# Performance work log

Measured on AMD Instinct MI355X. Metric: run time of the kernel, lower is better.

## Reference

```python
import jax, jax.numpy as jnp
import numpy as np

B, T, C, H = 16, 2048, 512, 4
DH = C // H  # head dim = 128


def setup_inputs() -> dict:
    key = jax.random.key(0)
    ks = jax.random.split(key, 12)
    s = 1.0 / np.sqrt(C).astype(np.float32)
    u = lambda k, shape: jax.random.uniform(k, shape, jnp.float32, -s, s)
    return {
        "x": jax.random.normal(ks[0], (B, C, 2, T), jnp.float32),
        "device_embedding": jax.random.normal(ks[1], (1, 2, C), jnp.float32),
        "in_proj_w": u(ks[2], (3 * C, C)),
        "in_proj_b": jnp.zeros((3 * C,), jnp.float32),
        "out_proj_w": u(ks[3], (C, C)),
        "out_proj_b": jnp.zeros((C,), jnp.float32),
        "phone_w": u(ks[4], (C, C)),
        "phone_b": u(ks[5], (C,)),
        "imu_w": u(ks[6], (C, C)),
        "imu_b": u(ks[7], (C,)),
        "output_w": u(ks[8], (C, 2 * C)),
        "output_b": u(ks[9], (C,)),
    }


def reference(x, device_embedding, in_proj_w, in_proj_b, out_proj_w, out_proj_b,
              phone_w, phone_b, imu_w, imu_b, output_w, output_b):
    Bx, Cx, Hdev, Tx = x.shape  # Hdev == 2 devices (phone, IMU)
    N = Bx * Tx
    # (B, C, 2, T) -> (B*T, 2, C), add learned device embedding
    xe = jnp.transpose(x, (0, 3, 2, 1)).reshape(N, 2, Cx) + device_embedding
    # torch nn.MultiheadAttention: packed in_proj, scale 1/sqrt(head_dim)
    wq, wk, wv = jnp.split(in_proj_w, 3, axis=0)
    bq, bk, bv = jnp.split(in_proj_b, 3, axis=0)
    to_heads = lambda t: t.reshape(N, 2, H, DH).transpose(0, 2, 1, 3)  # (N, H, 2, DH)
    q = to_heads(xe @ wq.T + bq)
    k = to_heads(xe @ wk.T + bk)
    v = to_heads(xe @ wv.T + bv)
    scores = jnp.einsum('nhqd,nhkd->nhqk', q, k) / jnp.float32(np.sqrt(DH))
    probs = jax.nn.softmax(scores, axis=-1)  # (N, H, 2, 2)
    ctx = jnp.einsum('nhqk,nhkd->nhqd', probs, v).transpose(0, 2, 1, 3).reshape(N, 2, Cx)
    attended = (ctx @ out_proj_w.T + out_proj_b).reshape(Bx, Tx, 2, Cx)
    phone = attended[:, :, 0, :] @ phone_w.T + phone_b
    imu = attended[:, :, 1, :] @ imu_w.T + imu_b
    out = jnp.concatenate([phone, imu], axis=-1) @ output_w.T + output_b  # (B, T, C)
    out = jnp.transpose(out, (0, 2, 1))  # (B, C, T)
    # head-averaged attention weights, then averaged over time
    avg_attention = probs.mean(axis=1).reshape(Bx, Tx, 2, 2).mean(axis=1)  # (B, 2, 2)
    return out, avg_attention
```

## Files before the change

kernel.cpp:

```cpp
#include <hip/hip_runtime.h>
#include <stdint.h>

typedef unsigned short u16;
typedef short short8 __attribute__((ext_vector_type(8)));
typedef float floatx4 __attribute__((ext_vector_type(4)));

__device__ __forceinline__ u16 f2bf(float f) {
  union { float f; unsigned u; } t; t.f = f;
  return (u16)((t.u + 0x7fffu + ((t.u >> 16) & 1u)) >> 16);
}
__device__ __forceinline__ float lo16(unsigned w) { union { unsigned u; float f; } t; t.u = w << 16; return t.f; }
__device__ __forceinline__ float hi16(unsigned w) { union { unsigned u; float f; } t; t.u = w & 0xffff0000u; return t.f; }
__device__ __forceinline__ void unpack8(uint4 v, float* f) {
  f[0]=lo16(v.x); f[1]=hi16(v.x); f[2]=lo16(v.y); f[3]=hi16(v.y);
  f[4]=lo16(v.z); f[5]=hi16(v.z); f[6]=lo16(v.w); f[7]=hi16(v.w);
}
__device__ __forceinline__ uint4 pack8(const u16* o) {
  uint4 v;
  v.x = (unsigned)o[0] | ((unsigned)o[1] << 16);
  v.y = (unsigned)o[2] | ((unsigned)o[3] << 16);
  v.z = (unsigned)o[4] | ((unsigned)o[5] << 16);
  v.w = (unsigned)o[6] | ((unsigned)o[7] << 16);
  return v;
}

__device__ __forceinline__ void gll16(const void* g, void* l) {
  __builtin_amdgcn_global_load_lds(
      (const __attribute__((address_space(1))) void*)(uintptr_t)(g),
      (__attribute__((address_space(3))) void*)(unsigned)(uintptr_t)(l),
      16, 0, 0);
}

__device__ __forceinline__ void cvt4(const float* s, u16* d, int g) {
  float4 v = *(const float4*)(s + (size_t)g * 4);
  ushort4 o; o.x = f2bf(v.x); o.y = f2bf(v.y); o.z = f2bf(v.z); o.w = f2bf(v.w);
  *(ushort4*)(d + (size_t)g * 4) = o;
}
__global__ __launch_bounds__(256)
void prep_convert(const float* __restrict__ inw, const float* __restrict__ phw,
                  const float* __restrict__ imw, const float* __restrict__ ow,
                  const float* __restrict__ outw,
                  u16* __restrict__ inw_bf, u16* __restrict__ phw_bf,
                  u16* __restrict__ imw_bf, u16* __restrict__ ow_bf,
                  u16* __restrict__ outwT) {
  int which = blockIdx.y;
  int g = blockIdx.x * 256 + threadIdx.x;
  if (which == 0) { if (g < 196608) cvt4(inw, inw_bf, g); }
  else if (which == 1) { if (g < 65536) cvt4(phw, phw_bf, g); }
  else if (which == 2) { if (g < 65536) cvt4(imw, imw_bf, g); }
  else if (which == 3) { if (g < 131072) cvt4(ow, ow_bf, g); }
  else {
    if (g < 65536) {
      int i0 = (g >> 9) * 4, j = g & 511;
      ushort4 o;
      o.x = f2bf(outw[(size_t)(i0 + 0) * 512 + j]);
      o.y = f2bf(outw[(size_t)(i0 + 1) * 512 + j]);
      o.z = f2bf(outw[(size_t)(i0 + 2) * 512 + j]);
      o.w = f2bf(outw[(size_t)(i0 + 3) * 512 + j]);
      outwT[(size_t)j * 512 + i0 + 0] = o.x;
      outwT[(size_t)j * 512 + i0 + 1] = o.y;
      outwT[(size_t)j * 512 + i0 + 2] = o.z;
      outwT[(size_t)j * 512 + i0 + 3] = o.w;
    }
  }
}

__global__ __launch_bounds__(256)
void uv_kernel(const float* __restrict__ phw, const float* __restrict__ phb,
               const float* __restrict__ imw, const float* __restrict__ imb,
               const float* __restrict__ outb, float* __restrict__ uv) {
  int g = blockIdx.x * 256 + threadIdx.x;
  int i = g & 511;
  const float* W = (g < 512) ? phw : imw;
  const float* bb = (g < 512) ? phb : imb;
  float s = bb[i];
#pragma unroll 4
  for (int c = 0; c < 512; ++c) s += W[(size_t)i * 512 + c] * outb[c];
  uv[g] = s;
}

__global__ __launch_bounds__(256)
void bcomb_kernel(const float* __restrict__ ow, const float* __restrict__ ob,
                  const float* __restrict__ uv, float* __restrict__ bcomb) {
  int i = blockIdx.x * 256 + threadIdx.x;
  float s = ob[i];
#pragma unroll 4
  for (int r = 0; r < 1024; ++r) s += ow[(size_t)i * 1024 + r] * uv[r];
  bcomb[i] = s;
}

__global__ __launch_bounds__(256)
void build_xe(const float* __restrict__ x, const float* __restrict__ emb,
              u16* __restrict__ xe) {
  __shared__ u16 tile[64][66];
  int bt = blockIdx.x;
  int tt = bt & 31, ct = (bt >> 5) & 7, d = (bt >> 8) & 1, b = bt >> 9;
  int t0 = tt * 64, c0 = ct * 64;
  int tid = threadIdx.x;
  int q = tid & 15, r = tid >> 4;
#pragma unroll
  for (int p = 0; p < 4; ++p) {
    int c = p * 16 + r;
    const float* src = x + ((size_t)((b * 512 + c0 + c) * 2 + d)) * 2048 + t0 + q * 4;
    float4 v = *(const float4*)src;
    float e = emb[d * 512 + c0 + c];
    ushort4 o; o.x = f2bf(v.x + e); o.y = f2bf(v.y + e); o.z = f2bf(v.z + e); o.w = f2bf(v.w + e);
    *(ushort4*)&tile[c][q * 4] = o;
  }
  __syncthreads();
  int cq = tid & 7, tp = tid >> 3;
  int cc0 = cq * 8;
  u16 o0[8], o1[8];
#pragma unroll
  for (int i = 0; i < 8; ++i) {
    unsigned w2 = *(const unsigned*)&tile[cc0 + i][2 * tp];
    o0[i] = (u16)(w2 & 0xffffu); o1[i] = (u16)(w2 >> 16);
  }
  size_t n = (size_t)b * 2048 + t0 + 2 * tp;
  *(uint4*)(xe + (n * 2 + d) * 512 + c0 + cc0) = pack8(o0);
  *(uint4*)(xe + ((n + 1) * 2 + d) * 512 + c0 + cc0) = pack8(o1);
}

template<int EPI>
__global__ __launch_bounds__(256, 3)
void gemm_bt(const u16* __restrict__ A, int lda,
             const u16* __restrict__ B, int ldb,
             const float* __restrict__ bias,
             void* __restrict__ Cv, int ldc, int K,
             const float* __restrict__ P) {
  __shared__ u16 As[128 * 64];
  __shared__ u16 Bs[128 * 64];
  int m0 = blockIdx.x * 128;
  int n0 = blockIdx.y * 128;
  int t = threadIdx.x;
  int lane = t & 63;
  int w = t >> 6;
  int wm = (w >> 1) * 64, wn = (w & 1) * 64;
  int l15 = lane & 15, quad = lane >> 4;

  floatx4 acc[4][4];
#pragma unroll
  for (int i = 0; i < 4; ++i)
#pragma unroll
    for (int j = 0; j < 4; ++j) acc[i][j] = (floatx4){0.f, 0.f, 0.f, 0.f};

  int lrow = lane >> 3, lcol = (lane & 7) * 8;
  const u16* gA = A + (size_t)(m0 + w * 32 + lrow) * lda + lcol;
  const u16* gB = B + (size_t)(n0 + w * 32 + lrow) * ldb + lcol;
  u16* lA = As + (w * 32) * 64;
  u16* lB = Bs + (w * 32) * 64;

  int KT = K >> 6;
  for (int kt = 0; kt < KT; ++kt) {
    int ko = kt * 64;
#pragma unroll
    for (int j = 0; j < 4; ++j) {
      gll16(gA + (size_t)(j * 8) * lda + ko, lA + (j * 8) * 64);
      gll16(gB + (size_t)(j * 8) * ldb + ko, lB + (j * 8) * 64);
    }
    __syncthreads();
#pragma unroll
    for (int ki = 0; ki < 2; ++ki) {
      short8 af[4], bfv[4];
#pragma unroll
      for (int i = 0; i < 4; ++i)
        af[i] = *(const short8*)&As[(wm + i * 16 + l15) * 64 + ki * 32 + quad * 8];
#pragma unroll
      for (int j = 0; j < 4; ++j)
        bfv[j] = *(const short8*)&Bs[(wn + j * 16 + l15) * 64 + ki * 32 + quad * 8];
#pragma unroll
      for (int i = 0; i < 4; ++i)
#pragma unroll
        for (int j = 0; j < 4; ++j)
          acc[i][j] = __builtin_amdgcn_mfma_f32_16x16x32_bf16(af[i], bfv[j], acc[i][j], 0, 0, 0);
    }
    __syncthreads();
  }

#pragma unroll
  for (int i = 0; i < 4; ++i) {
    int mrow = m0 + wm + i * 16 + quad * 4;
    float4 P0, P1;
    if (EPI == 2) {
      int np0 = mrow >> 1;
      P0 = *(const float4*)&P[((size_t)np0 * 4 + blockIdx.y) * 4];
      P1 = *(const float4*)&P[((size_t)(np0 + 1) * 4 + blockIdx.y) * 4];
    }
#pragma unroll
    for (int j = 0; j < 4; ++j) {
      int col = n0 + wn + j * 16 + l15;
      float bv = bias[col];
      floatx4 a = acc[i][j];
      if (EPI == 1) {
        int bb = mrow >> 11, ti = mrow & 2047;
        float4 o; o.x = a[0] + bv; o.y = a[1] + bv; o.z = a[2] + bv; o.w = a[3] + bv;
        *(float4*)&((float*)Cv)[((size_t)bb * ldc + col) * 2048 + ti] = o;
      } else if (EPI == 2) {
        float a0 = a[0] + bv, a1 = a[1] + bv, a2 = a[2] + bv, a3 = a[3] + bv;
        u16* C = (u16*)Cv;
        C[(size_t)(mrow + 0) * ldc + col] = f2bf(P0.x * a0 + P0.y * a1);
        C[(size_t)(mrow + 1) * ldc + col] = f2bf(P0.z * a0 + P0.w * a1);
        C[(size_t)(mrow + 2) * ldc + col] = f2bf(P1.x * a2 + P1.y * a3);
        C[(size_t)(mrow + 3) * ldc + col] = f2bf(P1.z * a2 + P1.w * a3);
      } else {
        u16* C = (u16*)Cv;
#pragma unroll
        for (int r = 0; r < 4; ++r)
          C[(size_t)(mrow + r) * ldc + col] = f2bf(a[r] + bv);
      }
    }
  }
}

__device__ __forceinline__ void compute_tile(const u16 (&Asr)[4][8192],
                                             const u16 (&Bsr)[4][8192],
                                             int bo, int aoff, int boff,
                                             floatx4 (&acc)[8][4]) {
  short8 af[8], bfv[4];
#pragma unroll
  for (int i = 0; i < 8; ++i)
    af[i] = *(const short8*)&Asr[bo][aoff + i * 512];
#pragma unroll
  for (int j = 0; j < 4; ++j)
    bfv[j] = *(const short8*)&Bsr[bo][boff + j * 512];
  __builtin_amdgcn_s_setprio(1);
#pragma unroll
  for (int i = 0; i < 8; ++i)
#pragma unroll
    for (int j = 0; j < 4; ++j)
      acc[i][j] = __builtin_amdgcn_mfma_f32_16x16x32_bf16(af[i], bfv[j], acc[i][j], 0, 0, 0);
  __builtin_amdgcn_s_setprio(0);
}

template<int EPI>
__global__ __launch_bounds__(512, 2)
void gemm256(const u16* __restrict__ A, int lda,
             const u16* __restrict__ B, int ldb,
             const float* __restrict__ bias,
             void* __restrict__ Cv, int ldc, int K,
             const float* __restrict__ P, int nbs) {
  __shared__ u16 As[4][8192];
  __shared__ u16 Bs[4][8192];
  int nwg = gridDim.x;
  int bid = blockIdx.x;
  int chunk = nwg >> 3;
  int g = (bid & 7) * chunk + (bid >> 3);
  int nb = g & ((1 << nbs) - 1), mb = g >> nbs;
  int m0 = mb * 256, n0 = nb * 256;
  int t = threadIdx.x;
  int lane = t & 63, w = t >> 6;
  int wr = w >> 2, wc = w & 3;
  int l15 = lane & 15, quad = lane >> 4;
  int wb = w * 512;
  int srow = t >> 2, sch = (t & 3) * 8;
  const u16* gA0 = A + (size_t)(m0 + srow) * lda + sch;
  const u16* gA1 = gA0 + (size_t)128 * lda;
  const u16* gB0 = B + (size_t)(n0 + srow) * ldb + sch;
  const u16* gB1 = gB0 + (size_t)128 * ldb;

  floatx4 acc[8][4];
#pragma unroll
  for (int i = 0; i < 8; ++i)
#pragma unroll
    for (int j = 0; j < 4; ++j) acc[i][j] = (floatx4){0.f, 0.f, 0.f, 0.f};

  int aoff = (wr * 128 + l15) * 32 + quad * 8;
  int boff = (wc * 64 + l15) * 32 + quad * 8;
  int KT = K >> 5;

#define STAGE256(ts) { int _b = (ts) & 3; int _ko = (ts) * 32;             \
    gll16(gA0 + _ko, (void*)&As[_b][wb]);                                  \
    gll16(gA1 + _ko, (void*)&As[_b][wb + 4096]);                           \
    gll16(gB0 + _ko, (void*)&Bs[_b][wb]);                                  \
    gll16(gB1 + _ko, (void*)&Bs[_b][wb + 4096]); }

  STAGE256(0)
  STAGE256(1)
  STAGE256(2)
  for (int tt = 0; tt < KT - 3; ++tt) {
    STAGE256(tt + 3)
    asm volatile("s_waitcnt vmcnt(12)" ::: "memory");
    asm volatile("s_barrier" ::: "memory");
    compute_tile(As, Bs, tt & 3, aoff, boff, acc);
    asm volatile("s_barrier" ::: "memory");
  }
  asm volatile("s_waitcnt vmcnt(8)" ::: "memory");
  asm volatile("s_barrier" ::: "memory");
  compute_tile(As, Bs, (KT - 3) & 3, aoff, boff, acc);
  asm volatile("s_waitcnt vmcnt(4)" ::: "memory");
  asm volatile("s_barrier" ::: "memory");
  compute_tile(As, Bs, (KT - 2) & 3, aoff, boff, acc);
  asm volatile("s_waitcnt vmcnt(0)" ::: "memory");
  asm volatile("s_barrier" ::: "memory");
  compute_tile(As, Bs, (KT - 1) & 3, aoff, boff, acc);
#undef STAGE256

#pragma unroll
  for (int i = 0; i < 8; ++i) {
    int mrow = m0 + wr * 128 + i * 16 + quad * 4;
#pragma unroll
    for (int j = 0; j < 4; ++j) {
      int col = n0 + wc * 64 + j * 16 + l15;
      float bv = bias[col];
      floatx4 a = acc[i][j];
      if (EPI == 1) {
        int bb = mrow >> 11, ti = mrow & 2047;
        float4 o; o.x = a[0] + bv; o.y = a[1] + bv; o.z = a[2] + bv; o.w = a[3] + bv;
        *(float4*)&((float*)Cv)[((size_t)bb * ldc + col) * 2048 + ti] = o;
      } else if (EPI == 2) {
        int np0 = mrow >> 1;
        int h = col >> 7;
        float4 P0 = *(const float4*)&P[((size_t)np0 * 4 + h) * 4];
        float4 P1 = *(const float4*)&P[((size_t)(np0 + 1) * 4 + h) * 4];
        float a0 = a[0] + bv, a1 = a[1] + bv, a2 = a[2] + bv, a3 = a[3] + bv;
        u16* C = (u16*)Cv;
        C[(size_t)(mrow + 0) * ldc + col] = f2bf(P0.x * a0 + P0.y * a1);
        C[(size_t)(mrow + 1) * ldc + col] = f2bf(P0.z * a0 + P0.w * a1);
        C[(size_t)(mrow + 2) * ldc + col] = f2bf(P1.x * a2 + P1.y * a3);
        C[(size_t)(mrow + 3) * ldc + col] = f2bf(P1.z * a2 + P1.w * a3);
      } else {
        u16* C = (u16*)Cv;
#pragma unroll
        for (int r = 0; r < 4; ++r)
          C[(size_t)(mrow + r) * ldc + col] = f2bf(a[r] + bv);
      }
    }
  }
}

__global__ __launch_bounds__(256)
void score_kernel(const u16* __restrict__ QK, float* __restrict__ P,
                  float* __restrict__ asum) {
  int g = blockIdx.x * 256 + threadIdx.x;
  int n = g >> 2, h = g & 3;
  const u16* q0 = QK + (size_t)(2 * n) * 1024 + h * 128;
  const u16* q1 = q0 + 1024;
  const u16* k0 = q0 + 512;
  const u16* k1 = k0 + 1024;

  float s00 = 0.f, s01 = 0.f, s10 = 0.f, s11 = 0.f;
#pragma unroll
  for (int c = 0; c < 128; c += 8) {
    float fq0[8], fq1[8], fk0[8], fk1[8];
    unpack8(*(const uint4*)(q0 + c), fq0);
    unpack8(*(const uint4*)(q1 + c), fq1);
    unpack8(*(const uint4*)(k0 + c), fk0);
    unpack8(*(const uint4*)(k1 + c), fk1);
#pragma unroll
    for (int u = 0; u < 8; ++u) {
      s00 += fq0[u] * fk0[u]; s01 += fq0[u] * fk1[u];
      s10 += fq1[u] * fk0[u]; s11 += fq1[u] * fk1[u];
    }
  }
  const float sc = 0.08838834764831845f;
  s00 *= sc; s01 *= sc; s10 *= sc; s11 *= sc;
  float m0v = fmaxf(s00, s01), m1v = fmaxf(s10, s11);
  float e00 = __expf(s00 - m0v), e01 = __expf(s01 - m0v);
  float e10 = __expf(s10 - m1v), e11 = __expf(s11 - m1v);
  float i0 = 1.f / (e00 + e01), i1 = 1.f / (e10 + e11);
  float4 p; p.x = e00 * i0; p.y = e01 * i0; p.z = e10 * i1; p.w = e11 * i1;
  *(float4*)&P[(size_t)g * 4] = p;

  float pv[4] = {p.x, p.y, p.z, p.w};
#pragma unroll
  for (int k2 = 0; k2 < 4; ++k2) {
    float v = pv[k2];
    v += __shfl_down(v, 32, 64); v += __shfl_down(v, 16, 64);
    v += __shfl_down(v, 8, 64);  v += __shfl_down(v, 4, 64);
    v += __shfl_down(v, 2, 64);  v += __shfl_down(v, 1, 64);
    pv[k2] = v;
  }
  __shared__ float red[4][4];
  int lane = threadIdx.x & 63, wv = threadIdx.x >> 6;
  if (lane == 0) { red[wv][0] = pv[0]; red[wv][1] = pv[1]; red[wv][2] = pv[2]; red[wv][3] = pv[3]; }
  __syncthreads();
  if (threadIdx.x < 4) {
    float s = red[0][threadIdx.x] + red[1][threadIdx.x] + red[2][threadIdx.x] + red[3][threadIdx.x];
    int b = (blockIdx.x * 64) >> 11;
    atomicAdd(&asum[b * 4 + threadIdx.x], s);
  }
}

__global__ void avg_kernel(const float* __restrict__ asum, float* __restrict__ out) {
  int i = threadIdx.x;
  out[16777216 + i] = asum[i] * (1.0f / 8192.0f);
}

extern "C" void kernel_launch(void* const* d_in, const int* in_sizes, int n_in,
                              void* d_out, int out_size, void* d_ws, size_t ws_size,
                              hipStream_t stream) {
  const float* x    = (const float*)d_in[0];
  const float* emb  = (const float*)d_in[1];
  const float* inw  = (const float*)d_in[2];
  const float* inb  = (const float*)d_in[3];
  const float* outw = (const float*)d_in[4];
  const float* outb = (const float*)d_in[5];
  const float* phw  = (const float*)d_in[6];
  const float* phb  = (const float*)d_in[7];
  const float* imw  = (const float*)d_in[8];
  const float* imb  = (const float*)d_in[9];
  const float* ow   = (const float*)d_in[10];
  const float* ob   = (const float*)d_in[11];
  float* outF = (float*)d_out;

  char* wsb = (char*)d_ws;
  u16*   ctx    = (u16*)wsb;
  u16*   QK     = (u16*)(wsb + 67108864);
  u16*   outwT  = (u16*)(wsb + 67108864);
  u16*   phw_bf = (u16*)(wsb + 67633152);
  u16*   imw_bf = (u16*)(wsb + 68157440);
  u16*   ow_bf  = (u16*)(wsb + 68681728);
  u16*   T1T    = (u16*)(wsb + 69730304);
  u16*   T2T    = (u16*)(wsb + 70254592);
  u16*   inw_bf = (u16*)(wsb + 201326592);
  u16*   Wcomb  = (u16*)(wsb + 202899456);
  float* uv     = (float*)(wsb + 203948032);
  float* bcomb  = (float*)(wsb + 203952128);
  float* P      = (float*)(wsb + 203954176);
  float* asum   = (float*)(wsb + 206051328);
  float* zbias  = (float*)(wsb + 206051584);
  u16*   xe     = (u16*)d_out;

  hipMemsetAsync(asum, 0, 2304, stream);

  build_xe<<<8192, 256, 0, stream>>>(x, emb, xe);

  prep_convert<<<dim3(768, 5), 256, 0, stream>>>(inw, phw, imw, ow, outw,
                                                 inw_bf, phw_bf, imw_bf, ow_bf, outwT);
  gemm_bt<0><<<dim3(4, 4), 256, 0, stream>>>(outwT, 512, phw_bf, 512, zbias, T1T, 512, 512, nullptr);
  gemm_bt<0><<<dim3(4, 4), 256, 0, stream>>>(outwT, 512, imw_bf, 512, zbias, T2T, 512, 512, nullptr);
  gemm_bt<0><<<dim3(4, 4), 256, 0, stream>>>(ow_bf, 1024, T1T, 512, zbias, Wcomb, 1024, 512, nullptr);
  gemm_bt<0><<<dim3(4, 4), 256, 0, stream>>>(ow_bf + 512, 1024, T2T, 512, zbias, Wcomb + 512, 1024, 512, nullptr);
  uv_kernel<<<4, 256, 0, stream>>>(phw, phb, imw, imb, outb, uv);
  bcomb_kernel<<<2, 256, 0, stream>>>(ow, ob, uv, bcomb);

  gemm256<0><<<1024, 512, 0, stream>>>(xe, 512, inw_bf, 512, inb,
                                       QK, 1024, 512, nullptr, 2);
  score_kernel<<<512, 256, 0, stream>>>(QK, P, asum);
  gemm256<2><<<512, 512, 0, stream>>>(xe, 512, inw_bf + 524288, 512,
                                      inb + 1024, ctx, 512, 512, P, 1);
  gemm256<1><<<256, 512, 0, stream>>>(ctx, 1024, Wcomb, 1024,
                                      bcomb, outF, 512, 1024, nullptr, 1);
  avg_kernel<<<1, 64, 0, stream>>>(asum, outF);
}
```

Baseline: 623.6 us.

## Split GEMM k-step into two half-phases interleaving LDS reads, prefetch and MFMA

The gemm256 main loop now splits each K tile into two halves. Each half loads its fragments from shared memory, issues one of the A or B global-to-LDS prefetches for tile tt+3, then runs 16 MFMAs at raised priority, with explicit barriers, lgkmcnt waits and sched_barriers between phases. Tail tiles are handled inside the same loop by stepping the vmcnt wait down. The goal is to overlap global prefetch and LDS traffic with matrix-core work and keep waves in lockstep. The cost is more barriers per iteration and tighter hand scheduling, which may stall if the phases are unbalanced.

```diff
diff --git a/kernel.cpp b/kernel.cpp
--- a/kernel.cpp
+++ b/kernel.cpp
@@ -212,26 +212,6 @@
   }
 }
 
-__device__ __forceinline__ void compute_tile(const u16 (&Asr)[4][8192],
-                                             const u16 (&Bsr)[4][8192],
-                                             int bo, int aoff, int boff,
-                                             floatx4 (&acc)[8][4]) {
-  short8 af[8], bfv[4];
-#pragma unroll
-  for (int i = 0; i < 8; ++i)
-    af[i] = *(const short8*)&Asr[bo][aoff + i * 512];
-#pragma unroll
-  for (int j = 0; j < 4; ++j)
-    bfv[j] = *(const short8*)&Bsr[bo][boff + j * 512];
-  __builtin_amdgcn_s_setprio(1);
-#pragma unroll
-  for (int i = 0; i < 8; ++i)
-#pragma unroll
-    for (int j = 0; j < 4; ++j)
-      acc[i][j] = __builtin_amdgcn_mfma_f32_16x16x32_bf16(af[i], bfv[j], acc[i][j], 0, 0, 0);
-  __builtin_amdgcn_s_setprio(0);
-}
-
 template<int EPI>
 __global__ __launch_bounds__(512, 2)
 void gemm256(const u16* __restrict__ A, int lda,
@@ -268,32 +248,63 @@
   int boff = (wc * 64 + l15) * 32 + quad * 8;
   int KT = K >> 5;
 
-#define STAGE256(ts) { int _b = (ts) & 3; int _ko = (ts) * 32;             \
+#define STA256(ts) { int _b = (ts) & 3; int _ko = (ts) * 32;               \
     gll16(gA0 + _ko, (void*)&As[_b][wb]);                                  \
-    gll16(gA1 + _ko, (void*)&As[_b][wb + 4096]);                           \
+    gll16(gA1 + _ko, (void*)&As[_b][wb + 4096]); }
+#define STB256(ts) { int _b = (ts) & 3; int _ko = (ts) * 32;               \
     gll16(gB0 + _ko, (void*)&Bs[_b][wb]);                                  \
     gll16(gB1 + _ko, (void*)&Bs[_b][wb + 4096]); }
 
-  STAGE256(0)
-  STAGE256(1)
-  STAGE256(2)
-  for (int tt = 0; tt < KT - 3; ++tt) {
-    STAGE256(tt + 3)
-    asm volatile("s_waitcnt vmcnt(12)" ::: "memory");
-    asm volatile("s_barrier" ::: "memory");
-    compute_tile(As, Bs, tt & 3, aoff, boff, acc);
-    asm volatile("s_barrier" ::: "memory");
-  }
+  STA256(0) STB256(0)
+  STA256(1) STB256(1)
+  STA256(2) STB256(2)
   asm volatile("s_waitcnt vmcnt(8)" ::: "memory");
   asm volatile("s_barrier" ::: "memory");
-  compute_tile(As, Bs, (KT - 3) & 3, aoff, boff, acc);
-  asm volatile("s_waitcnt vmcnt(4)" ::: "memory");
-  asm volatile("s_barrier" ::: "memory");
-  compute_tile(As, Bs, (KT - 2) & 3, aoff, boff, acc);
-  asm volatile("s_waitcnt vmcnt(0)" ::: "memory");
-  asm volatile("s_barrier" ::: "memory");
-  compute_tile(As, Bs, (KT - 1) & 3, aoff, boff, acc);
-#undef STAGE256
+
+  short8 af[8], bfv[4];
+  for (int tt = 0; tt < KT; ++tt) {
+    int bo = tt & 3;
+#pragma unroll
+    for (int i = 0; i < 4; ++i)
+      af[i] = *(const short8*)&As[bo][aoff + i * 512];
+#pragma unroll
+    for (int j = 0; j < 4; ++j)
+      bfv[j] = *(const short8*)&Bs[bo][boff + j * 512];
+    if (tt < KT - 3) STA256(tt + 3)
+    asm volatile("s_barrier" ::: "memory");
+    asm volatile("s_waitcnt lgkmcnt(0)" ::: "memory");
+    __builtin_amdgcn_sched_barrier(0);
+    __builtin_amdgcn_s_setprio(1);
+#pragma unroll
+    for (int i = 0; i < 4; ++i)
+#pragma unroll
+      for (int j = 0; j < 4; ++j)
+        acc[i][j] = __builtin_amdgcn_mfma_f32_16x16x32_bf16(af[i], bfv[j], acc[i][j], 0, 0, 0);
+    __builtin_amdgcn_s_setprio(0);
+    __builtin_amdgcn_sched_barrier(0);
+    asm volatile("s_barrier" ::: "memory");
+#pragma unroll
+    for (int i = 4; i < 8; ++i)
+      af[i] = *(const short8*)&As[bo][aoff + i * 512];
+    if (tt < KT - 3) STB256(tt + 3)
+    asm volatile("s_barrier" ::: "memory");
+    asm volatile("s_waitcnt lgkmcnt(0)" ::: "memory");
+    __builtin_amdgcn_sched_barrier(0);
+    __builtin_amdgcn_s_setprio(1);
+#pragma unroll
+    for (int i = 4; i < 8; ++i)
+#pragma unroll
+      for (int j = 0; j < 4; ++j)
+        acc[i][j] = __builtin_amdgcn_mfma_f32_16x16x32_bf16(af[i], bfv[j], acc[i][j], 0, 0, 0);
+    __builtin_amdgcn_s_setprio(0);
+    __builtin_amdgcn_sched_barrier(0);
+    if (tt < KT - 3)       { asm volatile("s_waitcnt vmcnt(8)" ::: "memory"); }
+    else if (tt == KT - 3) { asm volatile("s_waitcnt vmcnt(4)" ::: "memory"); }
+    else if (tt == KT - 2) { asm volatile("s_waitcnt vmcnt(0)" ::: "memory"); }
+    if (tt < KT - 1) asm volatile("s_barrier" ::: "memory");
+  }
+#undef STA256
+#undef STB256
 
 #pragma unroll
   for (int i = 0; i < 8; ++i) {
```

Result: no change. 618.5 us (-0.8%).
